# Kernel tuning notes

Measured on AMD Instinct MI355X. Metric: run time of the kernel, lower is better.

Reference implementation:

```python
import jax, jax.numpy as jnp
import numpy as np

EPS = 1e-6

def layernorm(x, alpha, bias):
    # torch.std default is unbiased (ddof=1)
    mean = x.mean(axis=-1, keepdims=True)
    std = jnp.std(x, axis=-1, keepdims=True, ddof=1)
    return alpha * (x - mean) / (std + EPS) + bias


def setup_inputs() -> dict:
    key = jax.random.key(0)
    B, L, d_model = 2, 1024, 1024
    d_state, d_conv, expand = 16, 4, 2
    d_inner = expand * d_model
    ks = jax.random.split(key, 8)
    std = 0.02
    x = jax.random.normal(ks[0], (B, L, d_model), dtype=jnp.float32)
    in_proj_w = jax.random.normal(ks[1], (2 * d_inner, d_model), dtype=jnp.float32) * std
    in_proj_b = jnp.zeros((2 * d_inner,), jnp.float32)
    conv_w = jax.random.normal(ks[2], (d_inner, 1, d_conv), dtype=jnp.float32) * std  # depthwise, groups=d_inner
    conv_b = jnp.zeros((d_inner,), jnp.float32)
    x_proj_w = jax.random.normal(ks[3], (2 * d_state, d_inner), dtype=jnp.float32) * std
    x_proj_b = jnp.zeros((2 * d_state,), jnp.float32)
    dt_proj_w = jax.random.normal(ks[4], (d_inner, d_inner), dtype=jnp.float32) * std
    dt_proj_b = jnp.zeros((d_inner,), jnp.float32)
    A_log = jnp.log(jnp.tile(jnp.arange(1, d_state + 1, dtype=jnp.float32), (d_inner, 1)))
    D = jnp.ones((d_inner,), jnp.float32)
    out_proj_w = jax.random.normal(ks[5], (d_model, d_inner), dtype=jnp.float32) * std
    out_proj_b = jnp.zeros((d_model,), jnp.float32)
    in_norm_alpha = jnp.ones((d_model,), jnp.float32)
    in_norm_bias = jnp.zeros((d_model,), jnp.float32)
    norm_alpha = jnp.ones((d_model,), jnp.float32)
    norm_bias = jnp.zeros((d_model,), jnp.float32)
    return {"x": x, "in_proj_w": in_proj_w, "in_proj_b": in_proj_b,
            "conv_w": conv_w, "conv_b": conv_b,
            "x_proj_w": x_proj_w, "x_proj_b": x_proj_b,
            "dt_proj_w": dt_proj_w, "dt_proj_b": dt_proj_b,
            "A_log": A_log, "D": D,
            "out_proj_w": out_proj_w, "out_proj_b": out_proj_b,
            "in_norm_alpha": in_norm_alpha, "in_norm_bias": in_norm_bias,
            "norm_alpha": norm_alpha, "norm_bias": norm_bias}


def reference(x, in_proj_w, in_proj_b, conv_w, conv_b, x_proj_w, x_proj_b,
              dt_proj_w, dt_proj_b, A_log, D, out_proj_w, out_proj_b,
              in_norm_alpha, in_norm_bias, norm_alpha, norm_bias):
    batch, L, d_model = x.shape
    d_inner = D.shape[0]
    d_state = A_log.shape[1]
    d_conv = conv_w.shape[-1]

    residual = x
    xn = layernorm(x, in_norm_alpha, in_norm_bias)
    xz = xn @ in_proj_w.T + in_proj_b                    # (B, L, 2*d_inner)
    x_in, z = jnp.split(xz, 2, axis=-1)

    # causal depthwise conv: torch pads both sides by d_conv-1 then slices [:L]
    # -> equivalent to left-pad only
    xc = jnp.swapaxes(x_in, 1, 2)                        # (B, d_inner, L)
    xc = jax.lax.conv_general_dilated(
        xc, conv_w, window_strides=(1,), padding=[(d_conv - 1, 0)],
        dimension_numbers=('NCH', 'OIH', 'NCH'),
        feature_group_count=d_inner) + conv_b[None, :, None]
    xc = jax.nn.silu(jnp.swapaxes(xc, 1, 2))             # (B, L, d_inner)

    Bmat, Cmat = jnp.split(xc @ x_proj_w.T + x_proj_b, 2, axis=-1)  # (B, L, d_state) each
    delta = jnp.clip(jax.nn.softplus(xc @ dt_proj_w.T + dt_proj_b), 1e-4, 10.0)
    A = -jnp.exp(A_log)                                  # (d_inner, d_state)
    flags = (jnp.arange(L) % 16) == 15                   # periodic renorm mask

    def step(h, inp):
        d_t, B_t, C_t, x_t, flag = inp                   # d_t,x_t: (B,d_inner); B_t,C_t: (B,d_state)
        dA = jnp.exp(jnp.clip(d_t[..., None] * A, -10.0, 0.0))      # (B,d_inner,d_state)
        dBx = d_t[..., None] * B_t[:, None, :] * x_t[..., None]
        h = dA * h + dBx
        hn = jnp.maximum(jnp.linalg.norm(h, axis=-1, keepdims=True), 1e-6)
        scale = jnp.where(hn > 10.0, 10.0 / hn, 1.0)
        h = jnp.where(flag, h * scale, h)
        y_t = jnp.sum(C_t[:, None, :] * h, axis=-1) + D * x_t
        return h, y_t

    h0 = jnp.zeros((batch, d_inner, d_state), dtype=x.dtype)
    xs = (jnp.swapaxes(delta, 0, 1), jnp.swapaxes(Bmat, 0, 1),
          jnp.swapaxes(Cmat, 0, 1), jnp.swapaxes(xc, 0, 1), flags)
    _, ys = jax.lax.scan(step, h0, xs)                   # ys: (L, B, d_inner)
    y = jnp.swapaxes(ys, 0, 1)

    y = y * jax.nn.silu(z)
    out = y @ out_proj_w.T + out_proj_b                  # dropout is identity in eval
    return layernorm(residual + out, norm_alpha, norm_bias)
```

## Files before the change

kernel.cpp:

```cpp
#include <hip/hip_runtime.h>
#include <math.h>

typedef unsigned short u16;
typedef unsigned int   u32;
typedef __bf16 bf16x8 __attribute__((ext_vector_type(8)));
typedef float  f32x4  __attribute__((ext_vector_type(4)));
typedef u16    u16x8  __attribute__((ext_vector_type(8)));

#define NB   2
#define LL   1024
#define DM   1024
#define DI   2048
#define MM   (NB*LL)
#define NXZ  (2*DI)
#define DSTATE 16
#define NSEG 64
#define NDT  2176
#define F32PAT 0x3F800000u

__device__ __forceinline__ float b2f(u16 u) {
  union { u32 i; float f; } v; v.i = ((u32)u) << 16; return v.f;
}
__device__ __forceinline__ u16 f2b(float f) {
  union { float f; u32 i; } v; v.f = f;
  u32 r = (v.i + 0x7FFFu + ((v.i >> 16) & 1u)) >> 16;
  return (u16)r;
}
__device__ __forceinline__ float ldx(const void* p, size_t i, bool isf32) {
  return isf32 ? ((const float*)p)[i] : b2f(((const u16*)p)[i]);
}

typedef __attribute__((address_space(1))) const void gas_t;
typedef __attribute__((address_space(3))) void las_t;
__device__ __forceinline__ void gload_lds16(const void* g, void* l) {
  __builtin_amdgcn_global_load_lds((gas_t*)g, (las_t*)l, 16, 0, 0);
}

__global__ __launch_bounds__(256) void ln1_kernel(
    const void* __restrict__ x, const void* __restrict__ alpha,
    const void* __restrict__ beta, u16* __restrict__ out,
    const u32* __restrict__ probe)
{
  const bool isf32 = (*probe == F32PAT);
  int row = blockIdx.x;
  int base = threadIdx.x * 4;
  size_t ix = (size_t)row * DM + base;
  float v0, v1, v2, v3;
  if (isf32) {
    float4 f = *(const float4*)((const float*)x + ix);
    v0 = f.x; v1 = f.y; v2 = f.z; v3 = f.w;
  } else {
    ushort4 u = *(const ushort4*)((const u16*)x + ix);
    v0 = b2f(u.x); v1 = b2f(u.y); v2 = b2f(u.z); v3 = b2f(u.w);
  }
  float s  = v0 + v1 + v2 + v3;
  float ss = v0*v0 + v1*v1 + v2*v2 + v3*v3;
#pragma unroll
  for (int off = 32; off > 0; off >>= 1) {
    s  += __shfl_down(s,  off);
    ss += __shfl_down(ss, off);
  }
  __shared__ float sb[4], ssb[4];
  int wv = threadIdx.x >> 6, ln = threadIdx.x & 63;
  if (ln == 0) { sb[wv] = s; ssb[wv] = ss; }
  __syncthreads();
  s  = sb[0]  + sb[1]  + sb[2]  + sb[3];
  ss = ssb[0] + ssb[1] + ssb[2] + ssb[3];
  float mean = s * (1.0f / DM);
  float var  = fmaxf((ss - (float)DM * mean * mean) * (1.0f / (DM - 1)), 0.0f);
  float inv  = 1.0f / (sqrtf(var) + 1e-6f);
  float a0 = ldx(alpha, base+0, isf32), a1 = ldx(alpha, base+1, isf32);
  float a2 = ldx(alpha, base+2, isf32), a3 = ldx(alpha, base+3, isf32);
  float b0 = ldx(beta,  base+0, isf32), b1 = ldx(beta,  base+1, isf32);
  float b2 = ldx(beta,  base+2, isf32), b3 = ldx(beta,  base+3, isf32);
  ushort4 o;
  o.x = f2b(a0 * (v0 - mean) * inv + b0);
  o.y = f2b(a1 * (v1 - mean) * inv + b1);
  o.z = f2b(a2 * (v2 - mean) * inv + b2);
  o.w = f2b(a3 * (v3 - mean) * inv + b3);
  *(ushort4*)(out + ix) = o;
}

__global__ __launch_bounds__(256) void ln2_kernel(
    const void* __restrict__ x, const float* __restrict__ outp,
    const void* __restrict__ alpha, const void* __restrict__ beta,
    void* __restrict__ out, const u32* __restrict__ probe)
{
  const bool isf32 = (*probe == F32PAT);
  int row = blockIdx.x;
  int base = threadIdx.x * 4;
  size_t ix = (size_t)row * DM + base;
  float v0, v1, v2, v3;
  if (isf32) {
    float4 f = *(const float4*)((const float*)x + ix);
    v0 = f.x; v1 = f.y; v2 = f.z; v3 = f.w;
  } else {
    ushort4 u = *(const ushort4*)((const u16*)x + ix);
    v0 = b2f(u.x); v1 = b2f(u.y); v2 = b2f(u.z); v3 = b2f(u.w);
  }
  float4 p = *(const float4*)(outp + ix);
  v0 += p.x; v1 += p.y; v2 += p.z; v3 += p.w;
  float s  = v0 + v1 + v2 + v3;
  float ss = v0*v0 + v1*v1 + v2*v2 + v3*v3;
#pragma unroll
  for (int off = 32; off > 0; off >>= 1) {
    s  += __shfl_down(s,  off);
    ss += __shfl_down(ss, off);
  }
  __shared__ float sb[4], ssb[4];
  int wv = threadIdx.x >> 6, ln = threadIdx.x & 63;
  if (ln == 0) { sb[wv] = s; ssb[wv] = ss; }
  __syncthreads();
  s  = sb[0]  + sb[1]  + sb[2]  + sb[3];
  ss = ssb[0] + ssb[1] + ssb[2] + ssb[3];
  float mean = s * (1.0f / DM);
  float var  = fmaxf((ss - (float)DM * mean * mean) * (1.0f / (DM - 1)), 0.0f);
  float inv  = 1.0f / (sqrtf(var) + 1e-6f);
  float a0 = ldx(alpha, base+0, isf32), a1 = ldx(alpha, base+1, isf32);
  float a2 = ldx(alpha, base+2, isf32), a3 = ldx(alpha, base+3, isf32);
  float b0 = ldx(beta,  base+0, isf32), b1 = ldx(beta,  base+1, isf32);
  float b2 = ldx(beta,  base+2, isf32), b3 = ldx(beta,  base+3, isf32);
  float r0 = a0 * (v0 - mean) * inv + b0;
  float r1 = a1 * (v1 - mean) * inv + b1;
  float r2 = a2 * (v2 - mean) * inv + b2;
  float r3 = a3 * (v3 - mean) * inv + b3;
  if (isf32) {
    float4 o; o.x = r0; o.y = r1; o.z = r2; o.w = r3;
    *(float4*)((float*)out + ix) = o;
  } else {
    ushort4 o; o.x = f2b(r0); o.y = f2b(r1); o.z = f2b(r2); o.w = f2b(r3);
    *(ushort4*)((u16*)out + ix) = o;
  }
}

#define CVT_A  4194304u
#define CVT_B  8388608u
#define CVT_C 10485760u
#define CVT_D 10551296u
#define CVT_E 10747904u

__global__ __launch_bounds__(256) void cvt_kernel(
    const void* __restrict__ s_in, const void* __restrict__ s_dt,
    const void* __restrict__ s_op, const void* __restrict__ s_xp,
    u16* __restrict__ inpw, u16* __restrict__ wdt, u16* __restrict__ opw,
    const u32* __restrict__ probe)
{
  const bool isf32 = (*probe == F32PAT);
  size_t i4 = ((size_t)blockIdx.x * 256 + threadIdx.x) * 4;
  if (i4 >= CVT_E) return;
  const void* src; u16* dst; size_t off;
  if      (i4 < CVT_A) { src = s_in; dst = inpw;              off = i4; }
  else if (i4 < CVT_B) { src = s_dt; dst = wdt;               off = i4 - CVT_A; }
  else if (i4 < CVT_C) { src = s_op; dst = opw;               off = i4 - CVT_B; }
  else if (i4 < CVT_D) { src = s_xp; dst = wdt + CVT_A;       off = i4 - CVT_C; }
  else {
    ushort4 z = {0, 0, 0, 0};
    *(ushort4*)(wdt + 4259840u + (i4 - CVT_D)) = z;
    return;
  }
  ushort4 o;
  if (isf32) {
    float4 f = *(const float4*)((const float*)src + off);
    o.x = f2b(f.x); o.y = f2b(f.y); o.z = f2b(f.z); o.w = f2b(f.w);
  } else {
    o = *(const ushort4*)((const u16*)src + off);
  }
  *(ushort4*)(dst + off) = o;
}

#define EPI_NONE 0
#define EPI_SOFTPLUS 1

template<int EPI, int OUTBF>
__global__ __launch_bounds__(256) void gemm_fast(
    const u16* __restrict__ A, const u16* __restrict__ W,
    const void* __restrict__ bias, void* __restrict__ Cout,
    const u32* __restrict__ probe, int M, int N, int K)
{
  __shared__ __align__(16) u16 As[128 * 32];
  __shared__ __align__(16) u16 Ws[128 * 32];
  const bool isf32 = (*probe == F32PAT);
  const int tid  = threadIdx.x;
  const int wave = tid >> 6;
  const int lane = tid & 63;
  const int quad = lane >> 4;
  const int l16  = lane & 15;
  const int m0 = blockIdx.x * 128;
  const int n0 = blockIdx.y * 128;
  const int wm = (wave >> 1) * 64;
  const int wn = (wave & 1) * 64;

  f32x4 acc[4][4] = {};

  for (int k0 = 0; k0 < K; k0 += 32) {
    __syncthreads();
#pragma unroll
    for (int q = 0; q < 2; ++q) {
      int ci  = wave * 128 + q * 64 + lane;
      int row = ci >> 2;
      int kc  = (ci & 3) * 8;
      const u16* ga = A + (size_t)(m0 + row) * K + k0 + kc;
      const u16* gw = W + (size_t)(n0 + row) * K + k0 + kc;
      u16* la = As + (size_t)(wave * 128 + q * 64) * 8;
      u16* lw = Ws + (size_t)(wave * 128 + q * 64) * 8;
      gload_lds16(ga, la);
      gload_lds16(gw, lw);
    }
    __syncthreads();
    bf16x8 af[4], bfr[4];
#pragma unroll
    for (int i = 0; i < 4; ++i) {
      af[i]  = *(const bf16x8*)(As + (size_t)(wm + i * 16 + l16) * 32 + quad * 8);
      bfr[i] = *(const bf16x8*)(Ws + (size_t)(wn + i * 16 + l16) * 32 + quad * 8);
    }
#pragma unroll
    for (int i = 0; i < 4; ++i)
#pragma unroll
      for (int j = 0; j < 4; ++j)
        acc[i][j] = __builtin_amdgcn_mfma_f32_16x16x32_bf16(af[i], bfr[j], acc[i][j], 0, 0, 0);
  }

#pragma unroll
  for (int i = 0; i < 4; ++i) {
    int rbase = m0 + wm + i * 16 + quad * 4;
#pragma unroll
    for (int j = 0; j < 4; ++j) {
      int col = n0 + wn + j * 16 + l16;
      float bv = ldx(bias, col, isf32);
#pragma unroll
      for (int r = 0; r < 4; ++r) {
        float v = acc[i][j][r] + bv;
        if (EPI == EPI_SOFTPLUS) {
          v = (v > 20.0f) ? v : __logf(1.0f + __expf(v));
          v = fminf(fmaxf(v, 1e-4f), 10.0f);
        }
        size_t oi = (size_t)(rbase + r) * N + col;
        if (OUTBF) ((u16*)Cout)[oi] = f2b(v);
        else       ((float*)Cout)[oi] = v;
      }
    }
  }
}

__global__ __launch_bounds__(256) void gemm_combo(
    const u16* __restrict__ A, const u16* __restrict__ W,
    const void* __restrict__ bias_dt, const void* __restrict__ bias_xp,
    float* __restrict__ delta, float* __restrict__ bc,
    const u32* __restrict__ probe, int K)
{
  __shared__ __align__(16) u16 As[128 * 32];
  __shared__ __align__(16) u16 Ws[128 * 32];
  const bool isf32 = (*probe == F32PAT);
  const int tid  = threadIdx.x;
  const int wave = tid >> 6;
  const int lane = tid & 63;
  const int quad = lane >> 4;
  const int l16  = lane & 15;
  const int m0 = blockIdx.x * 128;
  const int n0 = blockIdx.y * 128;
  const int wm = (wave >> 1) * 64;
  const int wn = (wave & 1) * 64;

  f32x4 acc[4][4] = {};

  for (int k0 = 0; k0 < K; k0 += 32) {
    __syncthreads();
#pragma unroll
    for (int q = 0; q < 2; ++q) {
      int ci  = wave * 128 + q * 64 + lane;
      int row = ci >> 2;
      int kc  = (ci & 3) * 8;
      const u16* ga = A + (size_t)(m0 + row) * K + k0 + kc;
      const u16* gw = W + (size_t)(n0 + row) * K + k0 + kc;
      u16* la = As + (size_t)(wave * 128 + q * 64) * 8;
      u16* lw = Ws + (size_t)(wave * 128 + q * 64) * 8;
      gload_lds16(ga, la);
      gload_lds16(gw, lw);
    }
    __syncthreads();
    bf16x8 af[4], bfr[4];
#pragma unroll
    for (int i = 0; i < 4; ++i) {
      af[i]  = *(const bf16x8*)(As + (size_t)(wm + i * 16 + l16) * 32 + quad * 8);
      bfr[i] = *(const bf16x8*)(Ws + (size_t)(wn + i * 16 + l16) * 32 + quad * 8);
    }
#pragma unroll
    for (int i = 0; i < 4; ++i)
#pragma unroll
      for (int j = 0; j < 4; ++j)
        acc[i][j] = __builtin_amdgcn_mfma_f32_16x16x32_bf16(af[i], bfr[j], acc[i][j], 0, 0, 0);
  }

#pragma unroll
  for (int i = 0; i < 4; ++i) {
    int rbase = m0 + wm + i * 16 + quad * 4;
#pragma unroll
    for (int j = 0; j < 4; ++j) {
      int col = n0 + wn + j * 16 + l16;
      if (col < DI) {
        float bv = ldx(bias_dt, col, isf32);
#pragma unroll
        for (int r = 0; r < 4; ++r) {
          float v = acc[i][j][r] + bv;
          v = (v > 20.0f) ? v : __logf(1.0f + __expf(v));
          v = fminf(fmaxf(v, 1e-4f), 10.0f);
          delta[(size_t)(rbase + r) * DI + col] = v;
        }
      } else if (col < DI + 32) {
        float bv = ldx(bias_xp, col - DI, isf32);
#pragma unroll
        for (int r = 0; r < 4; ++r)
          bc[(size_t)(rbase + r) * 32 + (col - DI)] = acc[i][j][r] + bv;
      }
    }
  }
}

template<int EPI, int OUTBF>
__global__ __launch_bounds__(256) void gemm_r2(
    const u16* __restrict__ A, const void* __restrict__ W,
    const void* __restrict__ bias, void* __restrict__ Cout,
    const u32* __restrict__ probe, int M, int N, int K)
{
  __shared__ __align__(16) u16 As[128 * 32];
  __shared__ __align__(16) u16 Ws[128 * 32];
  const bool isf32 = (*probe == F32PAT);
  const int tid  = threadIdx.x;
  const int wave = tid >> 6;
  const int lane = tid & 63;
  const int quad = lane >> 4;
  const int l16  = lane & 15;
  const int m0 = blockIdx.x * 128;
  const int n0 = blockIdx.y * 128;
  const int wm = (wave >> 1) * 64;
  const int wn = (wave & 1) * 64;

  f32x4 acc[4][4] = {};

  for (int k0 = 0; k0 < K; k0 += 32) {
    u16x8 va[2], vw[2];
#pragma unroll
    for (int q = 0; q < 2; ++q) {
      int ci  = wave * 128 + q * 64 + lane;
      int row = ci >> 2;
      int kc  = (ci & 3) * 8;
      va[q] = *(const u16x8*)(A + (size_t)(m0 + row) * K + k0 + kc);
      size_t wi = (size_t)(n0 + row) * K + k0 + kc;
      if (isf32) {
        const float* Wf = (const float*)W;
        float4 f0 = *(const float4*)(Wf + wi);
        float4 f1 = *(const float4*)(Wf + wi + 4);
        u16x8 t;
        t[0] = f2b(f0.x); t[1] = f2b(f0.y); t[2] = f2b(f0.z); t[3] = f2b(f0.w);
        t[4] = f2b(f1.x); t[5] = f2b(f1.y); t[6] = f2b(f1.z); t[7] = f2b(f1.w);
        vw[q] = t;
      } else {
        vw[q] = *(const u16x8*)((const u16*)W + wi);
      }
    }
    __syncthreads();
#pragma unroll
    for (int q = 0; q < 2; ++q) {
      int ci = wave * 128 + q * 64 + lane;
      *(u16x8*)(As + (size_t)ci * 8) = va[q];
      *(u16x8*)(Ws + (size_t)ci * 8) = vw[q];
    }
    __syncthreads();
    bf16x8 af[4], bfr[4];
#pragma unroll
    for (int i = 0; i < 4; ++i) {
      af[i]  = *(const bf16x8*)(As + (size_t)(wm + i * 16 + l16) * 32 + quad * 8);
      bfr[i] = *(const bf16x8*)(Ws + (size_t)(wn + i * 16 + l16) * 32 + quad * 8);
    }
#pragma unroll
    for (int i = 0; i < 4; ++i)
#pragma unroll
      for (int j = 0; j < 4; ++j)
        acc[i][j] = __builtin_amdgcn_mfma_f32_16x16x32_bf16(af[i], bfr[j], acc[i][j], 0, 0, 0);
  }

#pragma unroll
  for (int i = 0; i < 4; ++i) {
    int rbase = m0 + wm + i * 16 + quad * 4;
#pragma unroll
    for (int j = 0; j < 4; ++j) {
      int col = n0 + wn + j * 16 + l16;
      float bv = ldx(bias, col, isf32);
#pragma unroll
      for (int r = 0; r < 4; ++r) {
        float v = acc[i][j][r] + bv;
        if (EPI == EPI_SOFTPLUS) {
          v = (v > 20.0f) ? v : __logf(1.0f + __expf(v));
          v = fminf(fmaxf(v, 1e-4f), 10.0f);
        }
        size_t oi = (size_t)(rbase + r) * N + col;
        if (OUTBF) ((u16*)Cout)[oi] = f2b(v);
        else       ((float*)Cout)[oi] = v;
      }
    }
  }
}

__global__ __launch_bounds__(256) void conv_silu_kernel(
    const u16* __restrict__ xz, const void* __restrict__ cw,
    const void* __restrict__ cb, u16* __restrict__ xc_bf,
    const u32* __restrict__ probe)
{
  const bool isf32 = (*probe == F32PAT);
  int g = blockIdx.x * 256 + threadIdx.x;
  int c = g & (DI - 1);
  int m = g >> 11;
  int l = m & (LL - 1);
  float w0 = ldx(cw, c*4+0, isf32), w1 = ldx(cw, c*4+1, isf32);
  float w2 = ldx(cw, c*4+2, isf32), w3 = ldx(cw, c*4+3, isf32);
  const u16* col = xz + (size_t)m * NXZ + c;
  float acc = ldx(cb, c, isf32);
  acc += w3 * b2f(col[0]);
  if (l >= 1) acc += w2 * b2f(*(col - NXZ));
  if (l >= 2) acc += w1 * b2f(*(col - 2*NXZ));
  if (l >= 3) acc += w0 * b2f(*(col - 3*NXZ));
  float sil = acc / (1.0f + __expf(-acc));
  xc_bf[g] = f2b(sil);
}

__global__ __launch_bounds__(256) void proj_bc_r2(
    const u16* __restrict__ xc, const void* __restrict__ W,
    const void* __restrict__ bias, float* __restrict__ bc,
    const u32* __restrict__ probe)
{
  const bool isf32 = (*probe == F32PAT);
  int m = blockIdx.x;
  int n = threadIdx.x >> 3;
  int part = threadIdx.x & 7;
  const u16* xr = xc + (size_t)m * DI + part * 256;
  size_t wbase = (size_t)n * DI + part * 256;
  float acc = 0.0f;
  if (isf32) {
    const float* wr = (const float*)W + wbase;
#pragma unroll 8
    for (int i = 0; i < 256; i += 4) {
      ushort4 xv = *(const ushort4*)(xr + i);
      float4  wv = *(const float4*)(wr + i);
      acc += b2f(xv.x)*wv.x + b2f(xv.y)*wv.y + b2f(xv.z)*wv.z + b2f(xv.w)*wv.w;
    }
  } else {
    const u16* wr = (const u16*)W + wbase;
#pragma unroll 8
    for (int i = 0; i < 256; i += 4) {
      ushort4 xv = *(const ushort4*)(xr + i);
      ushort4 wv = *(const ushort4*)(wr + i);
      acc += b2f(xv.x)*b2f(wv.x) + b2f(xv.y)*b2f(wv.y)
           + b2f(xv.z)*b2f(wv.z) + b2f(xv.w)*b2f(wv.w);
    }
  }
  __shared__ float ps[256];
  ps[threadIdx.x] = acc;
  __syncthreads();
  if (threadIdx.x < 32) {
    float s = 0.0f;
#pragma unroll
    for (int p = 0; p < 8; ++p) s += ps[threadIdx.x * 8 + p];
    bc[(size_t)m * 32 + threadIdx.x] = s + ldx(bias, threadIdx.x, isf32);
  }
}


__global__ __launch_bounds__(256, 4) void scan_p1(
    const float* __restrict__ delta, const float* __restrict__ bc,
    const u16* __restrict__ xc, const void* __restrict__ A_log,
    float2* __restrict__ PQ, const u32* __restrict__ probe)
{
  const bool isf32 = (*probe == F32PAT);
  const int c = blockIdx.x * 256 + threadIdx.x;
  const int g = blockIdx.y;
  const int b = blockIdx.z;
  const int row0 = b * LL + g * 16;
  __shared__ float sBC[512];
  if (threadIdx.x < 128)
    *(float4*)&sBC[threadIdx.x * 4] =
        *(const float4*)(bc + (size_t)row0 * 32 + threadIdx.x * 4);
  float Av2[16];
#pragma unroll
  for (int s = 0; s < 16; ++s)
    Av2[s] = -__expf(ldx(A_log, (size_t)c * DSTATE + s, isf32)) * 1.44269504f;
  float p[16], q[16];
#pragma unroll
  for (int s = 0; s < 16; ++s) { p[s] = 1.0f; q[s] = 0.0f; }
  __syncthreads();
  const float CLIP2 = -14.4269504f;
#pragma unroll 4
  for (int j = 0; j < 16; ++j) {
    int row = row0 + j;
    float d  = delta[(size_t)row * DI + c];
    float x  = b2f(xc[(size_t)row * DI + c]);
    float dx = d * x;
    float4 B4[4];
    B4[0] = *(const float4*)&sBC[j * 32 + 0];
    B4[1] = *(const float4*)&sBC[j * 32 + 4];
    B4[2] = *(const float4*)&sBC[j * 32 + 8];
    B4[3] = *(const float4*)&sBC[j * 32 + 12];
    const float* Bv = (const float*)B4;
#pragma unroll
    for (int s = 0; s < 16; ++s) {
      float a = __builtin_amdgcn_exp2f(fmaxf(d * Av2[s], CLIP2));
      q[s] = a * q[s] + dx * Bv[s];
      p[s] *= a;
    }
  }
  float2* out = PQ + ((size_t)(b * NSEG + g) * DI + c) * DSTATE;
#pragma unroll
  for (int s = 0; s < 16; ++s) out[s] = make_float2(p[s], q[s]);
}

__global__ __launch_bounds__(256) void scan_p2(
    const float2* __restrict__ PQ, float* __restrict__ Hin,
    float* __restrict__ Scale)
{
  const int s = threadIdx.x & 15;
  const int c = blockIdx.x * 16 + (threadIdx.x >> 4);
  const int b = blockIdx.y;
  const size_t stride = (size_t)DI * DSTATE;
  const size_t base = ((size_t)b * NSEG * DI + c) * DSTATE + s;
  float h = 0.0f;
  float2 pq = PQ[base];
  for (int g = 0; g < NSEG; ++g) {
    float2 cur = pq;
    if (g < NSEG - 1) pq = PQ[base + (size_t)(g + 1) * stride];
    Hin[base + (size_t)g * stride] = h;
    h = cur.x * h + cur.y;
    float n2 = h * h;
    n2 += __shfl_xor(n2, 1);
    n2 += __shfl_xor(n2, 2);
    n2 += __shfl_xor(n2, 4);
    n2 += __shfl_xor(n2, 8);
    float hn = fmaxf(sqrtf(n2), 1e-6f);
    float sc = hn > 10.0f ? 10.0f / hn : 1.0f;
    if (s == 0) Scale[((size_t)b * NSEG + g) * DI + c] = sc;
    h *= sc;
  }
}

__global__ __launch_bounds__(256, 4) void scan_p3(
    const float* __restrict__ delta, const float* __restrict__ bc,
    const u16* __restrict__ xc, const u16* __restrict__ xz,
    const void* __restrict__ A_log, const void* __restrict__ Dp,
    const float* __restrict__ Hin, const float* __restrict__ Scale,
    u16* __restrict__ y_bf, const u32* __restrict__ probe)
{
  const bool isf32 = (*probe == F32PAT);
  const int c = blockIdx.x * 256 + threadIdx.x;
  const int g = blockIdx.y;
  const int b = blockIdx.z;
  const int row0 = b * LL + g * 16;
  __shared__ float sBC[512];
  if (threadIdx.x < 128)
    *(float4*)&sBC[threadIdx.x * 4] =
        *(const float4*)(bc + (size_t)row0 * 32 + threadIdx.x * 4);
  float Av2[16];
#pragma unroll
  for (int s = 0; s < 16; ++s)
    Av2[s] = -__expf(ldx(A_log, (size_t)c * DSTATE + s, isf32)) * 1.44269504f;
  float h[16];
  const float* hp = Hin + ((size_t)(b * NSEG + g) * DI + c) * DSTATE;
#pragma unroll
  for (int s4 = 0; s4 < 4; ++s4)
    *(float4*)&h[s4 * 4] = *(const float4*)(hp + s4 * 4);
  const float sc15 = Scale[((size_t)b * NSEG + g) * DI + c];
  const float Dc = ldx(Dp, c, isf32);
  __syncthreads();
  const float CLIP2 = -14.4269504f;
#pragma unroll 4
  for (int j = 0; j < 16; ++j) {
    int row = row0 + j;
    float d  = delta[(size_t)row * DI + c];
    float x  = b2f(xc[(size_t)row * DI + c]);
    float z  = b2f(xz[(size_t)row * NXZ + DI + c]);
    float dx = d * x;
    float4 BC[8];
    BC[0] = *(const float4*)&sBC[j * 32 + 0];
    BC[1] = *(const float4*)&sBC[j * 32 + 4];
    BC[2] = *(const float4*)&sBC[j * 32 + 8];
    BC[3] = *(const float4*)&sBC[j * 32 + 12];
    BC[4] = *(const float4*)&sBC[j * 32 + 16];
    BC[5] = *(const float4*)&sBC[j * 32 + 20];
    BC[6] = *(const float4*)&sBC[j * 32 + 24];
    BC[7] = *(const float4*)&sBC[j * 32 + 28];
    const float* Bv = (const float*)BC;
    const float* Cv = Bv + 16;
#pragma unroll
    for (int s = 0; s < 16; ++s) {
      float a = __builtin_amdgcn_exp2f(fmaxf(d * Av2[s], CLIP2));
      h[s] = a * h[s] + dx * Bv[s];
    }
    if (j == 15) {
#pragma unroll
      for (int s = 0; s < 16; ++s) h[s] *= sc15;
    }
    float ys = 0.0f;
#pragma unroll
    for (int s = 0; s < 16; ++s) ys += Cv[s] * h[s];
    float yo = (ys + Dc * x) * (z / (1.0f + __expf(-z)));
    y_bf[(size_t)row * DI + c] = f2b(yo);
  }
}

__global__ __launch_bounds__(256) void scan_mono(
    const float* __restrict__ delta, const float* __restrict__ bc,
    const u16* __restrict__ xc, const u16* __restrict__ xz,
    const void* __restrict__ A_log, const void* __restrict__ Dp,
    u16* __restrict__ y_bf, const u32* __restrict__ probe)
{
  const bool isf32 = (*probe == F32PAT);
  const int s = threadIdx.x & 15;
  const int c = blockIdx.x * 16 + (threadIdx.x >> 4);
  const int b = blockIdx.y;
  const float Av2 = -__expf(ldx(A_log, (size_t)c * DSTATE + s, isf32)) * 1.44269504f;
  const float Dc  = ldx(Dp, c, isf32);
  const float CLIP2 = -14.4269504f;
  float h = 0.0f;
  for (int t0 = 0; t0 < LL; t0 += 16) {
    float dl[16], xl[16], zl[16], Bv[16], Cv[16];
#pragma unroll
    for (int j = 0; j < 16; ++j) {
      int row = b * LL + t0 + j;
      dl[j] = delta[(size_t)row * DI + c];
      xl[j] = b2f(xc[(size_t)row * DI + c]);
      zl[j] = b2f(xz[(size_t)row * NXZ + DI + c]);
      Bv[j] = bc[(size_t)row * 32 + s];
      Cv[j] = bc[(size_t)row * 32 + 16 + s];
    }
#pragma unroll
    for (int j = 0; j < 16; ++j) {
      float d = dl[j], x = xl[j];
      float dA = __builtin_amdgcn_exp2f(fmaxf(d * Av2, CLIP2));
      h = dA * h + (d * x) * Bv[j];
      if (j == 15) {
        float n2 = h * h;
        n2 += __shfl_xor(n2, 1); n2 += __shfl_xor(n2, 2);
        n2 += __shfl_xor(n2, 4); n2 += __shfl_xor(n2, 8);
        float hn = fmaxf(sqrtf(n2), 1e-6f);
        float sc = hn > 10.0f ? 10.0f / hn : 1.0f;
        h *= sc;
      }
      float ys = Cv[j] * h;
      ys += __shfl_xor(ys, 1); ys += __shfl_xor(ys, 2);
      ys += __shfl_xor(ys, 4); ys += __shfl_xor(ys, 8);
      float z = zl[j];
      float yo = (ys + Dc * x) * (z / (1.0f + __expf(-z)));
      if (s == 0) {
        int row = b * LL + t0 + j;
        y_bf[(size_t)row * DI + c] = f2b(yo);
      }
    }
  }
}

extern "C" void kernel_launch(void* const* d_in, const int* in_sizes, int n_in,
                              void* d_out, int out_size, void* d_ws, size_t ws_size,
                              hipStream_t stream) {
  const void* x          = d_in[0];
  const void* in_proj_w  = d_in[1];
  const void* in_proj_b  = d_in[2];
  const void* conv_w     = d_in[3];
  const void* conv_b     = d_in[4];
  const void* x_proj_w   = d_in[5];
  const void* x_proj_b   = d_in[6];
  const void* dt_proj_w  = d_in[7];
  const void* dt_proj_b  = d_in[8];
  const void* A_log      = d_in[9];
  const void* Dp         = d_in[10];
  const void* out_proj_w = d_in[11];
  const void* out_proj_b = d_in[12];
  const void* in_norm_a  = d_in[13];
  const void* in_norm_b  = d_in[14];
  const void* norm_a     = d_in[15];
  const void* norm_b     = d_in[16];
  const u32*  probe      = (const u32*)d_in[13];

  const size_t MiB = 1048576;
  const size_t NEED_NEW = 106299392;

  if (ws_size >= NEED_NEW) {
    char* w = (char*)d_ws;
    u16*   xz_bf = (u16*)w;    w += 16 * MiB;
    u16*   xc_bf = (u16*)w;    w += 8 * MiB;
    float* delta = (float*)w;  w += 16 * MiB;
    float* bc    = (float*)w;  w += 256 * 1024;
    float* Scale = (float*)w;  w += 1 * MiB;
    u16*   opw   = (u16*)w;    w += 4 * MiB;
    u16*   y_bf  = (u16*)w;    w += 8 * MiB;
    float* Hin   = (float*)w;  w += 16 * MiB;
    char*  R32   = w;          w += 32 * MiB;
    u16*    inpw  = (u16*)(R32);
    u16*    wdt   = (u16*)(R32 + 8 * MiB);
    u16*    xn_bf = (u16*)(R32 + 16 * MiB + 512 * 1024);
    float2* PQ    = (float2*)R32;
    float*  outp  = (float*)R32;

    cvt_kernel<<<10496, 256, 0, stream>>>(in_proj_w, dt_proj_w, out_proj_w, x_proj_w,
                                          inpw, wdt, opw, probe);
    ln1_kernel<<<MM, 256, 0, stream>>>(x, in_norm_a, in_norm_b, xn_bf, probe);
    gemm_fast<EPI_NONE, 1><<<dim3(MM/128, NXZ/128), 256, 0, stream>>>(
        xn_bf, inpw, in_proj_b, xz_bf, probe, MM, NXZ, DM);
    conv_silu_kernel<<<(MM * DI) / 256, 256, 0, stream>>>(xz_bf, conv_w, conv_b, xc_bf, probe);
    gemm_combo<<<dim3(MM/128, NDT/128), 256, 0, stream>>>(
        xc_bf, wdt, dt_proj_b, x_proj_b, delta, bc, probe, DI);
    scan_p1<<<dim3(DI/256, NSEG, NB), 256, 0, stream>>>(delta, bc, xc_bf, A_log, PQ, probe);
    scan_p2<<<dim3(DI/16, NB), 256, 0, stream>>>(PQ, Hin, Scale);
    scan_p3<<<dim3(DI/256, NSEG, NB), 256, 0, stream>>>(
        delta, bc, xc_bf, xz_bf, A_log, Dp, Hin, Scale, y_bf, probe);
    gemm_fast<EPI_NONE, 0><<<dim3(MM/128, DM/128), 256, 0, stream>>>(
        y_bf, opw, out_proj_b, outp, probe, MM, DM, DI);
    ln2_kernel<<<MM, 256, 0, stream>>>(x, outp, norm_a, norm_b, d_out, probe);
  } else {
    char* w = (char*)d_ws;
    u16*   xn_bf = (u16*)w;   w += (size_t)MM * DM * 2;
    u16*   xz_bf = (u16*)w;   w += (size_t)MM * NXZ * 2;
    u16*   xc_bf = (u16*)w;   w += (size_t)MM * DI * 2;
    float* delta = (float*)w; w += (size_t)MM * DI * 4;
    float* bc    = (float*)w; w += (size_t)MM * 32 * 4;
    u16*   y_bf  = (u16*)w;   w += (size_t)MM * DI * 2;
    float* outp  = (float*)w; w += (size_t)MM * DM * 4;

    ln1_kernel<<<MM, 256, 0, stream>>>(x, in_norm_a, in_norm_b, xn_bf, probe);
    gemm_r2<EPI_NONE, 1><<<dim3(MM/128, NXZ/128), 256, 0, stream>>>(
        xn_bf, in_proj_w, in_proj_b, xz_bf, probe, MM, NXZ, DM);
    conv_silu_kernel<<<(MM * DI) / 256, 256, 0, stream>>>(xz_bf, conv_w, conv_b, xc_bf, probe);
    gemm_r2<EPI_SOFTPLUS, 0><<<dim3(MM/128, DI/128), 256, 0, stream>>>(
        xc_bf, dt_proj_w, dt_proj_b, delta, probe, MM, DI, DI);
    proj_bc_r2<<<MM, 256, 0, stream>>>(xc_bf, x_proj_w, x_proj_b, bc, probe);
    scan_mono<<<dim3(DI/16, NB), 256, 0, stream>>>(delta, bc, xc_bf, xz_bf, A_log, Dp, y_bf, probe);
    gemm_r2<EPI_NONE, 0><<<dim3(MM/128, DM/128), 256, 0, stream>>>(
        y_bf, out_proj_w, out_proj_b, outp, probe, MM, DM, DI);
    ln2_kernel<<<MM, 256, 0, stream>>>(x, outp, norm_a, norm_b, d_out, probe);
  }
}
```

Baseline: 374.4 us.

## Split-K the dt/x projection and out_proj GEMMs with fused reduce epilogues

The combined dt/x projection GEMM now splits K in two and writes fp32 partials; a new reduce kernel sums them and applies bias, softplus and clamping. The out_proj GEMM splits K in four, and a new LayerNorm kernel sums the four partials, the bias and the residual before normalising. This targets the small grids (16x17 and 16x8 tiles) that underfill the GPU's many compute units, at the cost of extra fp32 partial traffic and one more launch. The workspace layout is reshuffled to fit the partial buffers.

```diff
diff --git a/kernel.cpp b/kernel.cpp
--- a/kernel.cpp
+++ b/kernel.cpp
@@ -133,6 +133,66 @@
   }
 }
 
+__global__ __launch_bounds__(256) void ln2_sk_kernel(
+    const void* __restrict__ x, const float* __restrict__ P,
+    const void* __restrict__ op_bias,
+    const void* __restrict__ alpha, const void* __restrict__ beta,
+    void* __restrict__ out, const u32* __restrict__ probe)
+{
+  const bool isf32 = (*probe == F32PAT);
+  int row = blockIdx.x;
+  int base = threadIdx.x * 4;
+  size_t ix = (size_t)row * DM + base;
+  float v0, v1, v2, v3;
+  if (isf32) {
+    float4 f = *(const float4*)((const float*)x + ix);
+    v0 = f.x; v1 = f.y; v2 = f.z; v3 = f.w;
+  } else {
+    ushort4 u = *(const ushort4*)((const u16*)x + ix);
+    v0 = b2f(u.x); v1 = b2f(u.y); v2 = b2f(u.z); v3 = b2f(u.w);
+  }
+  v0 += ldx(op_bias, base+0, isf32);
+  v1 += ldx(op_bias, base+1, isf32);
+  v2 += ldx(op_bias, base+2, isf32);
+  v3 += ldx(op_bias, base+3, isf32);
+#pragma unroll
+  for (int sk = 0; sk < 4; ++sk) {
+    float4 p = *(const float4*)(P + ((size_t)sk * MM + row) * DM + base);
+    v0 += p.x; v1 += p.y; v2 += p.z; v3 += p.w;
+  }
+  float s  = v0 + v1 + v2 + v3;
+  float ss = v0*v0 + v1*v1 + v2*v2 + v3*v3;
+#pragma unroll
+  for (int off = 32; off > 0; off >>= 1) {
+    s  += __shfl_down(s,  off);
+    ss += __shfl_down(ss, off);
+  }
+  __shared__ float sb[4], ssb[4];
+  int wv = threadIdx.x >> 6, ln = threadIdx.x & 63;
+  if (ln == 0) { sb[wv] = s; ssb[wv] = ss; }
+  __syncthreads();
+  s  = sb[0]  + sb[1]  + sb[2]  + sb[3];
+  ss = ssb[0] + ssb[1] + ssb[2] + ssb[3];
+  float mean = s * (1.0f / DM);
+  float var  = fmaxf((ss - (float)DM * mean * mean) * (1.0f / (DM - 1)), 0.0f);
+  float inv  = 1.0f / (sqrtf(var) + 1e-6f);
+  float a0 = ldx(alpha, base+0, isf32), a1 = ldx(alpha, base+1, isf32);
+  float a2 = ldx(alpha, base+2, isf32), a3 = ldx(alpha, base+3, isf32);
+  float b0 = ldx(beta,  base+0, isf32), b1 = ldx(beta,  base+1, isf32);
+  float b2 = ldx(beta,  base+2, isf32), b3 = ldx(beta,  base+3, isf32);
+  float r0 = a0 * (v0 - mean) * inv + b0;
+  float r1 = a1 * (v1 - mean) * inv + b1;
+  float r2 = a2 * (v2 - mean) * inv + b2;
+  float r3 = a3 * (v3 - mean) * inv + b3;
+  if (isf32) {
+    float4 o; o.x = r0; o.y = r1; o.z = r2; o.w = r3;
+    *(float4*)((float*)out + ix) = o;
+  } else {
+    ushort4 o; o.x = f2b(r0); o.y = f2b(r1); o.z = f2b(r2); o.w = f2b(r3);
+    *(ushort4*)((u16*)out + ix) = o;
+  }
+}
+
 #define CVT_A  4194304u
 #define CVT_B  8388608u
 #define CVT_C 10485760u
@@ -149,10 +209,10 @@
   size_t i4 = ((size_t)blockIdx.x * 256 + threadIdx.x) * 4;
   if (i4 >= CVT_E) return;
   const void* src; u16* dst; size_t off;
-  if      (i4 < CVT_A) { src = s_in; dst = inpw;              off = i4; }
-  else if (i4 < CVT_B) { src = s_dt; dst = wdt;               off = i4 - CVT_A; }
-  else if (i4 < CVT_C) { src = s_op; dst = opw;               off = i4 - CVT_B; }
-  else if (i4 < CVT_D) { src = s_xp; dst = wdt + CVT_A;       off = i4 - CVT_C; }
+  if      (i4 < CVT_A) { src = s_in; dst = inpw;        off = i4; }
+  else if (i4 < CVT_B) { src = s_dt; dst = wdt;         off = i4 - CVT_A; }
+  else if (i4 < CVT_C) { src = s_op; dst = opw;         off = i4 - CVT_B; }
+  else if (i4 < CVT_D) { src = s_xp; dst = wdt + CVT_A; off = i4 - CVT_C; }
   else {
     ushort4 z = {0, 0, 0, 0};
     *(ushort4*)(wdt + 4259840u + (i4 - CVT_D)) = z;
@@ -242,15 +302,12 @@
   }
 }
 
-__global__ __launch_bounds__(256) void gemm_combo(
+__global__ __launch_bounds__(256) void gemm_sk(
     const u16* __restrict__ A, const u16* __restrict__ W,
-    const void* __restrict__ bias_dt, const void* __restrict__ bias_xp,
-    float* __restrict__ delta, float* __restrict__ bc,
-    const u32* __restrict__ probe, int K)
+    float* __restrict__ P, int M, int N, int Kfull, int Kslice)
 {
   __shared__ __align__(16) u16 As[128 * 32];
   __shared__ __align__(16) u16 Ws[128 * 32];
-  const bool isf32 = (*probe == F32PAT);
   const int tid  = threadIdx.x;
   const int wave = tid >> 6;
   const int lane = tid & 63;
@@ -258,20 +315,23 @@
   const int l16  = lane & 15;
   const int m0 = blockIdx.x * 128;
   const int n0 = blockIdx.y * 128;
+  const int sk = blockIdx.z;
+  const int kbeg = sk * Kslice;
+  const int kend = kbeg + Kslice;
   const int wm = (wave >> 1) * 64;
   const int wn = (wave & 1) * 64;
 
   f32x4 acc[4][4] = {};
 
-  for (int k0 = 0; k0 < K; k0 += 32) {
+  for (int k0 = kbeg; k0 < kend; k0 += 32) {
     __syncthreads();
 #pragma unroll
     for (int q = 0; q < 2; ++q) {
       int ci  = wave * 128 + q * 64 + lane;
       int row = ci >> 2;
       int kc  = (ci & 3) * 8;
-      const u16* ga = A + (size_t)(m0 + row) * K + k0 + kc;
-      const u16* gw = W + (size_t)(n0 + row) * K + k0 + kc;
+      const u16* ga = A + (size_t)(m0 + row) * Kfull + k0 + kc;
+      const u16* gw = W + (size_t)(n0 + row) * Kfull + k0 + kc;
       u16* la = As + (size_t)(wave * 128 + q * 64) * 8;
       u16* lw = Ws + (size_t)(wave * 128 + q * 64) * 8;
       gload_lds16(ga, la);
@@ -291,27 +351,38 @@
         acc[i][j] = __builtin_amdgcn_mfma_f32_16x16x32_bf16(af[i], bfr[j], acc[i][j], 0, 0, 0);
   }
 
+  float* Pb = P + (size_t)sk * M * N;
 #pragma unroll
   for (int i = 0; i < 4; ++i) {
     int rbase = m0 + wm + i * 16 + quad * 4;
 #pragma unroll
     for (int j = 0; j < 4; ++j) {
       int col = n0 + wn + j * 16 + l16;
-      if (col < DI) {
-        float bv = ldx(bias_dt, col, isf32);
-#pragma unroll
-        for (int r = 0; r < 4; ++r) {
-          float v = acc[i][j][r] + bv;
-          v = (v > 20.0f) ? v : __logf(1.0f + __expf(v));
-          v = fminf(fmaxf(v, 1e-4f), 10.0f);
-          delta[(size_t)(rbase + r) * DI + col] = v;
-        }
-      } else if (col < DI + 32) {
-        float bv = ldx(bias_xp, col - DI, isf32);
-#pragma unroll
-        for (int r = 0; r < 4; ++r)
-          bc[(size_t)(rbase + r) * 32 + (col - DI)] = acc[i][j][r] + bv;
-      }
+#pragma unroll
+      for (int r = 0; r < 4; ++r)
+        Pb[(size_t)(rbase + r) * N + col] = acc[i][j][r];
+    }
+  }
+}
+
+__global__ __launch_bounds__(256) void reduce_combo(
+    const float* __restrict__ P, const void* __restrict__ bias_dt,
+    const void* __restrict__ bias_xp, float* __restrict__ delta,
+    float* __restrict__ bc, const u32* __restrict__ probe)
+{
+  const bool isf32 = (*probe == F32PAT);
+  const int m = blockIdx.x;
+  const float* p0 = P + (size_t)m * NDT;
+  const float* p1 = P + (size_t)(MM + m) * NDT;
+  for (int n = threadIdx.x; n < DI + 32; n += 256) {
+    float v = p0[n] + p1[n];
+    if (n < DI) {
+      v += ldx(bias_dt, n, isf32);
+      v = (v > 20.0f) ? v : __logf(1.0f + __expf(v));
+      v = fminf(fmaxf(v, 1e-4f), 10.0f);
+      delta[(size_t)m * DI + n] = v;
+    } else {
+      bc[(size_t)m * 32 + (n - DI)] = v + ldx(bias_xp, n - DI, isf32);
     }
   }
 }
@@ -463,7 +534,6 @@
     bc[(size_t)m * 32 + threadIdx.x] = s + ldx(bias, threadIdx.x, isf32);
   }
 }
-
 
 __global__ __launch_bounds__(256, 4) void scan_p1(
     const float* __restrict__ delta, const float* __restrict__ bc,
@@ -689,13 +759,14 @@
     float* Scale = (float*)w;  w += 1 * MiB;
     u16*   opw   = (u16*)w;    w += 4 * MiB;
     u16*   y_bf  = (u16*)w;    w += 8 * MiB;
-    float* Hin   = (float*)w;  w += 16 * MiB;
-    char*  R32   = w;          w += 32 * MiB;
-    u16*    inpw  = (u16*)(R32);
-    u16*    wdt   = (u16*)(R32 + 8 * MiB);
-    u16*    xn_bf = (u16*)(R32 + 16 * MiB + 512 * 1024);
-    float2* PQ    = (float2*)R32;
-    float*  outp  = (float*)R32;
+    char* S = w;
+    u16*    wdt    = (u16*)(S);
+    u16*    inpw   = (u16*)(S + 8*MiB + 512*1024);
+    u16*    xn_bf  = (u16*)(S + 16*MiB + 512*1024);
+    float*  deltaP = (float*)(S + 8*MiB + 512*1024);
+    float2* PQ     = (float2*)(S);
+    float*  Hin    = (float*)(S + 32*MiB);
+    float*  outP   = (float*)(S);
 
     cvt_kernel<<<10496, 256, 0, stream>>>(in_proj_w, dt_proj_w, out_proj_w, x_proj_w,
                                           inpw, wdt, opw, probe);
@@ -703,15 +774,16 @@
     gemm_fast<EPI_NONE, 1><<<dim3(MM/128, NXZ/128), 256, 0, stream>>>(
         xn_bf, inpw, in_proj_b, xz_bf, probe, MM, NXZ, DM);
     conv_silu_kernel<<<(MM * DI) / 256, 256, 0, stream>>>(xz_bf, conv_w, conv_b, xc_bf, probe);
-    gemm_combo<<<dim3(MM/128, NDT/128), 256, 0, stream>>>(
-        xc_bf, wdt, dt_proj_b, x_proj_b, delta, bc, probe, DI);
+    gemm_sk<<<dim3(MM/128, NDT/128, 2), 256, 0, stream>>>(
+        xc_bf, wdt, deltaP, MM, NDT, DI, DI/2);
+    reduce_combo<<<MM, 256, 0, stream>>>(deltaP, dt_proj_b, x_proj_b, delta, bc, probe);
     scan_p1<<<dim3(DI/256, NSEG, NB), 256, 0, stream>>>(delta, bc, xc_bf, A_log, PQ, probe);
     scan_p2<<<dim3(DI/16, NB), 256, 0, stream>>>(PQ, Hin, Scale);
     scan_p3<<<dim3(DI/256, NSEG, NB), 256, 0, stream>>>(
         delta, bc, xc_bf, xz_bf, A_log, Dp, Hin, Scale, y_bf, probe);
-    gemm_fast<EPI_NONE, 0><<<dim3(MM/128, DM/128), 256, 0, stream>>>(
-        y_bf, opw, out_proj_b, outp, probe, MM, DM, DI);
-    ln2_kernel<<<MM, 256, 0, stream>>>(x, outp, norm_a, norm_b, d_out, probe);
+    gemm_sk<<<dim3(MM/128, DM/128, 4), 256, 0, stream>>>(
+        y_bf, opw, outP, MM, DM, DI, DI/4);
+    ln2_sk_kernel<<<MM, 256, 0, stream>>>(x, outP, out_proj_b, norm_a, norm_b, d_out, probe);
   } else {
     char* w = (char*)d_ws;
     u16*   xn_bf = (u16*)w;   w += (size_t)MM * DM * 2;
```

New measurement: 346.6 us. 1.08x faster.
